# Kernel tuning notes

Hardware: AMD Instinct MI355X
Metric: run time of the kernel (lower is better)

## Reference

```python
import jax, jax.numpy as jnp
import numpy as np

N_NODES = 100000
N_EDGES = 800000
N_GRAPHS = 512          # 256 (query, corpus) pairs
NODE_FEAT, EDGE_FEAT = 16, 8
NODE_STATE, EDGE_STATE = 32, 16
MSG_H = 32              # message MLP hidden/out
UPD_H = 64              # node-update MLP hidden
GSTATE = 64             # graph embedding dim
N_PROP = 3
P = 1                   # int(output_mode[-1])
NODE_INS = NODE_DEL = 1.0


def _init_linear(key, fan_in, fan_out):
    s = 1.0 / np.sqrt(fan_in)
    kw, kb = jax.random.split(key)
    w = jax.random.uniform(kw, (fan_in, fan_out), jnp.float32, -s, s)
    b = jax.random.uniform(kb, (fan_out,), jnp.float32, -s, s)
    return w, b


def setup_inputs() -> dict:
    key = jax.random.key(0)
    ks = jax.random.split(key, 16)
    inp = {
        'node_features': jax.random.normal(ks[0], (N_NODES, NODE_FEAT), jnp.float32),
        'edge_features': jax.random.normal(ks[1], (N_EDGES, EDGE_FEAT), jnp.float32),
        'from_idx': jax.random.randint(ks[2], (N_EDGES,), 0, N_NODES, jnp.int32),
        'to_idx': jax.random.randint(ks[3], (N_EDGES,), 0, N_NODES, jnp.int32),
        'graph_idx': jnp.sort(jax.random.randint(ks[4], (N_NODES,), 0, N_GRAPHS, jnp.int32)),
    }
    # encoder (single linear layer MLPs, as in gmngen.GraphEncoder)
    inp['enc_node_w'], inp['enc_node_b'] = _init_linear(ks[5], NODE_FEAT, NODE_STATE)
    inp['enc_edge_w'], inp['enc_edge_b'] = _init_linear(ks[6], EDGE_FEAT, EDGE_STATE)
    # shared message net (reverse_dir_param_different=False): in = 2*node_state + edge_state
    inp['msg_w1'], inp['msg_b1'] = _init_linear(ks[7], 2 * NODE_STATE + EDGE_STATE, MSG_H)
    inp['msg_w2'], inp['msg_b2'] = _init_linear(ks[8], MSG_H, MSG_H)
    # residual node-update MLP: in = concat[agg_messages, node_states]
    inp['upd_w1'], inp['upd_b1'] = _init_linear(ks[9], MSG_H + NODE_STATE, UPD_H)
    inp['upd_w2'], inp['upd_b2'] = _init_linear(ks[10], UPD_H, NODE_STATE)
    # gated aggregator: MLP1 -> 2*GSTATE, MLP2: GSTATE -> GSTATE
    inp['agg_w1'], inp['agg_b1'] = _init_linear(ks[11], NODE_STATE, 2 * GSTATE)
    inp['agg_w2'], inp['agg_b2'] = _init_linear(ks[12], GSTATE, GSTATE)
    return inp


def _mlp2(x, w1, b1, w2, b2):
    return jax.nn.relu(x @ w1 + b1) @ w2 + b2


def reference(node_features, edge_features, from_idx, to_idx, graph_idx,
              enc_node_w, enc_node_b, enc_edge_w, enc_edge_b,
              msg_w1, msg_b1, msg_w2, msg_b2,
              upd_w1, upd_b1, upd_w2, upd_b2,
              agg_w1, agg_b1, agg_w2, agg_b2):
    # encoder
    h = node_features @ enc_node_w + enc_node_b              # [N, NODE_STATE]
    e = edge_features @ enc_edge_w + enc_edge_b              # [E, EDGE_STATE]

    for _ in range(N_PROP):
        fs = h[from_idx]                                     # [E, NODE_STATE]
        ts = h[to_idx]
        # forward-direction messages, scattered to to_idx
        m_f = _mlp2(jnp.concatenate([fs, ts, e], -1), msg_w1, msg_b1, msg_w2, msg_b2)
        agg = jax.ops.segment_sum(m_f, to_idx, num_segments=N_NODES)
        # reverse-direction messages (shared params), scattered to from_idx
        m_r = _mlp2(jnp.concatenate([ts, fs, e], -1), msg_w1, msg_b1, msg_w2, msg_b2)
        agg = agg + jax.ops.segment_sum(m_r, from_idx, num_segments=N_NODES)
        # residual node update: MLP(concat[messages, node_states]) + node_states
        h = h + _mlp2(jnp.concatenate([agg, h], -1), upd_w1, upd_b1, upd_w2, upd_b2)

    # gated aggregator
    g = h @ agg_w1 + agg_b1                                  # [N, 2*GSTATE]
    gated = jax.nn.sigmoid(g[:, :GSTATE]) * g[:, GSTATE:]
    graph_states = jax.ops.segment_sum(gated, graph_idx, num_segments=N_GRAPHS)
    graph_vectors = graph_states @ agg_w2 + agg_b2           # [G, GSTATE]

    # reshape_and_split_tensor(graph_vectors, 2): x = even rows, y = odd rows
    pairs = graph_vectors.reshape(-1, 2 * GSTATE)
    x, y = pairs[:, :GSTATE], pairs[:, GSTATE:]

    # asymm hinge norm, p = 1
    ins = jnp.sum(jax.nn.relu(y - x) ** P, axis=-1)
    dele = jnp.sum(jax.nn.relu(x - y) ** P, axis=-1)
    return NODE_INS * ins + NODE_DEL * dele                  # [G // 2]
```

## Files before the change

kernel.cpp:

```cpp
#include <hip/hip_runtime.h>
#include <math.h>

#define NN 100000
#define NE 800000
#define NG 512
#define NENT (2*NE)
#define NB ((NN + 1023)/1024)

__global__ __launch_bounds__(64) void k_prep(
    const float* __restrict__ ew, const float* __restrict__ eb,
    const float* __restrict__ mw1, const float* __restrict__ mb1,
    float* __restrict__ Wef, float* __restrict__ bef)
{
    int c = threadIdx.x;
    if (c >= 32) return;
    float bacc = mb1[c];
    for (int t = 0; t < 16; ++t) bacc = fmaf(eb[t], mw1[(64 + t) * 32 + c], bacc);
    bef[c] = bacc;
    for (int j = 0; j < 8; ++j) {
        float acc = 0.f;
        for (int t = 0; t < 16; ++t) acc = fmaf(ew[j * 16 + t], mw1[(64 + t) * 32 + c], acc);
        Wef[j * 32 + c] = acc;
    }
}

__global__ __launch_bounds__(256) void k_enc_nodes(
    const float* __restrict__ nf, const float* __restrict__ w,
    const float* __restrict__ bb, const float* __restrict__ mw1,
    float* __restrict__ h, float* __restrict__ A, float* __restrict__ B)
{
    int n = blockIdx.x * 256 + threadIdx.x;
    if (n >= NN) return;
    const float4* px = (const float4*)(nf + (size_t)n * 16);
    float4 x[4];
#pragma unroll
    for (int i = 0; i < 4; ++i) x[i] = px[i];
    float out[32];
#pragma unroll
    for (int j = 0; j < 32; ++j) out[j] = bb[j];
#pragma unroll
    for (int i = 0; i < 4; ++i) {
#pragma unroll
        for (int j = 0; j < 32; ++j) {
            out[j] = fmaf(x[i].x, w[(4*i+0)*32 + j], out[j]);
            out[j] = fmaf(x[i].y, w[(4*i+1)*32 + j], out[j]);
            out[j] = fmaf(x[i].z, w[(4*i+2)*32 + j], out[j]);
            out[j] = fmaf(x[i].w, w[(4*i+3)*32 + j], out[j]);
        }
    }
    float4* po = (float4*)(h + (size_t)n * 32);
#pragma unroll
    for (int j = 0; j < 8; ++j)
        po[j] = make_float4(out[4*j], out[4*j+1], out[4*j+2], out[4*j+3]);

    float Av[32], Bv[32];
#pragma unroll
    for (int c = 0; c < 32; ++c) { Av[c] = 0.f; Bv[c] = 0.f; }
#pragma unroll
    for (int i = 0; i < 32; ++i) {
        float r = out[i];
        const float* wra = mw1 + (size_t)i * 32;
        const float* wrb = mw1 + (size_t)(32 + i) * 32;
#pragma unroll
        for (int c = 0; c < 32; ++c) {
            Av[c] = fmaf(r, wra[c], Av[c]);
            Bv[c] = fmaf(r, wrb[c], Bv[c]);
        }
    }
    float4* pA = (float4*)(A + (size_t)n * 32);
    float4* pB = (float4*)(B + (size_t)n * 32);
#pragma unroll
    for (int j = 0; j < 8; ++j) {
        pA[j] = make_float4(Av[4*j], Av[4*j+1], Av[4*j+2], Av[4*j+3]);
        pB[j] = make_float4(Bv[4*j], Bv[4*j+1], Bv[4*j+2], Bv[4*j+3]);
    }
}

__global__ __launch_bounds__(256) void k_count(
    const int* __restrict__ fi, const int* __restrict__ ti, int* __restrict__ deg)
{
    int e = blockIdx.x * 256 + threadIdx.x;
    if (e >= NE) return;
    atomicAdd(&deg[ti[e]], 1);
    atomicAdd(&deg[fi[e]], 1);
}

__global__ __launch_bounds__(256) void k_scan1(
    const int* __restrict__ deg, int* __restrict__ offs, int* __restrict__ bsum)
{
    __shared__ int s[256];
    int b = blockIdx.x, t = threadIdx.x;
    int base = b * 1024 + t * 4;
    int v[4];
#pragma unroll
    for (int i = 0; i < 4; ++i) { int g = base + i; v[i] = (g < NN) ? deg[g] : 0; }
    int tsum = v[0] + v[1] + v[2] + v[3];
    s[t] = tsum;
    __syncthreads();
    for (int d = 1; d < 256; d <<= 1) {
        int xv = (t >= d) ? s[t - d] : 0;
        __syncthreads();
        s[t] += xv;
        __syncthreads();
    }
    int run = s[t] - tsum;
#pragma unroll
    for (int i = 0; i < 4; ++i) { int g = base + i; if (g < NN) offs[g] = run; run += v[i]; }
    if (t == 255) bsum[b] = s[255];
}

__global__ __launch_bounds__(128) void k_scan2(int* __restrict__ bsum, int nb)
{
    __shared__ int s[128];
    int t = threadIdx.x;
    int v = (t < nb) ? bsum[t] : 0;
    s[t] = v;
    __syncthreads();
    for (int d = 1; d < 128; d <<= 1) {
        int xv = (t >= d) ? s[t - d] : 0;
        __syncthreads();
        s[t] += xv;
        __syncthreads();
    }
    if (t < nb) bsum[t] = s[t] - v;
}

__global__ __launch_bounds__(256) void k_scan3(
    int* __restrict__ offs, const int* __restrict__ bsum, int* __restrict__ cursor)
{
    int g = blockIdx.x * 256 + threadIdx.x;
    if (g >= NN) return;
    int o = offs[g] + bsum[g >> 10];
    offs[g] = o;
    cursor[g] = o;
}

#define FILL_GROUPS 8
#define FILL_SUBBLK 256
#define RANGE_W (NN / FILL_GROUPS)
__global__ __launch_bounds__(256) void k_fill(
    const int* __restrict__ fi, const int* __restrict__ ti,
    int* __restrict__ cursor, int2* __restrict__ eplist)
{
    int grp = blockIdx.x & (FILL_GROUPS - 1);
    int sub = blockIdx.x >> 3;
    int lo = grp * RANGE_W;
    int hi = lo + RANGE_W;
    for (int e = sub * 256 + threadIdx.x; e < NE; e += FILL_SUBBLK * 256) {
        int f = fi[e], t = ti[e];
        if (t >= lo && t < hi) {
            int p = atomicAdd(&cursor[t], 1);
            eplist[p] = make_int2(e, f);
        }
        if (f >= lo && f < hi) {
            int p = atomicAdd(&cursor[f], 1);
            eplist[p] = make_int2(e, t);
        }
    }
}

__global__ __launch_bounds__(256) void k_gather(
    const int* __restrict__ offs, const int* __restrict__ deg,
    const int2* __restrict__ eplist,
    const float* __restrict__ A, const float* __restrict__ B,
    const float* __restrict__ ef,
    const float* __restrict__ Wef, const float* __restrict__ bef,
    float* __restrict__ aggH)
{
    int wave = (blockIdx.x * 256 + threadIdx.x) >> 6;
    if (wave >= NN) return;
    int lane = threadIdx.x & 63;
    int half = lane >> 5;
    int c = lane & 31;
    float w[8];
#pragma unroll
    for (int j = 0; j < 8; ++j) w[j] = Wef[j * 32 + c];
    float kbase = B[(size_t)wave * 32 + c] + bef[c];
    int beg = offs[wave];
    int end = beg + deg[wave];
    float acc0 = 0.f, acc1 = 0.f;
    int i = beg + half;
    for (; i + 2 < end; i += 4) {
        int2 ep0 = eplist[i];
        int2 ep1 = eplist[i + 2];
        float a0 = A[(size_t)ep0.y * 32 + c];
        float a1 = A[(size_t)ep1.y * 32 + c];
        const float4* pf0 = (const float4*)(ef + (size_t)ep0.x * 8);
        const float4* pf1 = (const float4*)(ef + (size_t)ep1.x * 8);
        float4 e00 = pf0[0], e01 = pf0[1];
        float4 e10 = pf1[0], e11 = pf1[1];
        float s0 = kbase + a0;
        s0 = fmaf(e00.x, w[0], s0); s0 = fmaf(e00.y, w[1], s0);
        s0 = fmaf(e00.z, w[2], s0); s0 = fmaf(e00.w, w[3], s0);
        s0 = fmaf(e01.x, w[4], s0); s0 = fmaf(e01.y, w[5], s0);
        s0 = fmaf(e01.z, w[6], s0); s0 = fmaf(e01.w, w[7], s0);
        float s1 = kbase + a1;
        s1 = fmaf(e10.x, w[0], s1); s1 = fmaf(e10.y, w[1], s1);
        s1 = fmaf(e10.z, w[2], s1); s1 = fmaf(e10.w, w[3], s1);
        s1 = fmaf(e11.x, w[4], s1); s1 = fmaf(e11.y, w[5], s1);
        s1 = fmaf(e11.z, w[6], s1); s1 = fmaf(e11.w, w[7], s1);
        acc0 += fmaxf(s0, 0.f);
        acc1 += fmaxf(s1, 0.f);
    }
    for (; i < end; i += 2) {
        int2 ep = eplist[i];
        float a = A[(size_t)ep.y * 32 + c];
        const float4* pf = (const float4*)(ef + (size_t)ep.x * 8);
        float4 f0 = pf[0], f1 = pf[1];
        float s = kbase + a;
        s = fmaf(f0.x, w[0], s); s = fmaf(f0.y, w[1], s);
        s = fmaf(f0.z, w[2], s); s = fmaf(f0.w, w[3], s);
        s = fmaf(f1.x, w[4], s); s = fmaf(f1.y, w[5], s);
        s = fmaf(f1.z, w[6], s); s = fmaf(f1.w, w[7], s);
        acc0 += fmaxf(s, 0.f);
    }
    float acc = acc0 + acc1;
    acc += __shfl_down(acc, 32);
    if (lane < 32) aggH[(size_t)wave * 32 + c] = acc;
}

__global__ __launch_bounds__(256) void k_update(
    const float* __restrict__ aggH, const int* __restrict__ deg,
    float* __restrict__ h,
    const float* __restrict__ mw2, const float* __restrict__ mb2,
    const float* __restrict__ uw1, const float* __restrict__ ub1,
    const float* __restrict__ uw2, const float* __restrict__ ub2,
    const float* __restrict__ mw1,
    float* __restrict__ A, float* __restrict__ B, int last)
{
    int n = blockIdx.x * 256 + threadIdx.x;
    if (n >= NN) return;
    float dg = (float)deg[n];
    float agg[32];
#pragma unroll
    for (int k = 0; k < 32; ++k) agg[k] = dg * mb2[k];
    {
        const float4* pa = (const float4*)(aggH + (size_t)n * 32);
#pragma unroll
        for (int i = 0; i < 8; ++i) {
            float4 v = pa[i];
            const float* wr0 = mw2 + (size_t)(4*i) * 32;
#pragma unroll
            for (int k = 0; k < 32; ++k) {
                float t0 = fmaf(v.x, wr0[k],      agg[k]);
                t0 = fmaf(v.y, wr0[32 + k], t0);
                t0 = fmaf(v.z, wr0[64 + k], t0);
                t0 = fmaf(v.w, wr0[96 + k], t0);
                agg[k] = t0;
            }
        }
    }
    float4* ph = (float4*)(h + (size_t)n * 32);
    float hv[32];
#pragma unroll
    for (int i = 0; i < 8; ++i) {
        float4 v = ph[i];
        hv[4*i] = v.x; hv[4*i+1] = v.y; hv[4*i+2] = v.z; hv[4*i+3] = v.w;
    }
    float out[32];
#pragma unroll
    for (int k = 0; k < 32; ++k) out[k] = ub2[k];
#pragma unroll
    for (int cB = 0; cB < 2; ++cB) {
        float hid[32];
#pragma unroll
        for (int j = 0; j < 32; ++j) hid[j] = ub1[cB * 32 + j];
#pragma unroll
        for (int i = 0; i < 32; ++i) {
            float r = agg[i];
            const float* wr = uw1 + (size_t)i * 64 + cB * 32;
#pragma unroll
            for (int j = 0; j < 32; ++j) hid[j] = fmaf(r, wr[j], hid[j]);
        }
#pragma unroll
        for (int i = 0; i < 32; ++i) {
            float r = hv[i];
            const float* wr = uw1 + (size_t)(32 + i) * 64 + cB * 32;
#pragma unroll
            for (int j = 0; j < 32; ++j) hid[j] = fmaf(r, wr[j], hid[j]);
        }
#pragma unroll
        for (int j = 0; j < 32; ++j) {
            float r = fmaxf(hid[j], 0.f);
            const float* wr = uw2 + (size_t)(cB * 32 + j) * 32;
#pragma unroll
            for (int k = 0; k < 32; ++k) out[k] = fmaf(r, wr[k], out[k]);
        }
    }
#pragma unroll
    for (int k = 0; k < 32; ++k) hv[k] += out[k];
#pragma unroll
    for (int i = 0; i < 8; ++i)
        ph[i] = make_float4(hv[4*i], hv[4*i+1], hv[4*i+2], hv[4*i+3]);

    if (!last) {
        float Av[32], Bv[32];
#pragma unroll
        for (int c = 0; c < 32; ++c) { Av[c] = 0.f; Bv[c] = 0.f; }
#pragma unroll
        for (int i = 0; i < 32; ++i) {
            float r = hv[i];
            const float* wra = mw1 + (size_t)i * 32;
            const float* wrb = mw1 + (size_t)(32 + i) * 32;
#pragma unroll
            for (int c = 0; c < 32; ++c) {
                Av[c] = fmaf(r, wra[c], Av[c]);
                Bv[c] = fmaf(r, wrb[c], Bv[c]);
            }
        }
        float4* pA = (float4*)(A + (size_t)n * 32);
        float4* pB = (float4*)(B + (size_t)n * 32);
#pragma unroll
        for (int j = 0; j < 8; ++j) {
            pA[j] = make_float4(Av[4*j], Av[4*j+1], Av[4*j+2], Av[4*j+3]);
            pB[j] = make_float4(Bv[4*j], Bv[4*j+1], Bv[4*j+2], Bv[4*j+3]);
        }
    }
}

#define FN_WAVES 4096
#define FN_CHUNK ((NN + FN_WAVES - 1) / FN_WAVES)
__global__ __launch_bounds__(256) void k_final_nodes(
    const float* __restrict__ h, const int* __restrict__ gidx,
    const float* __restrict__ w1, const float* __restrict__ b1,
    float* __restrict__ gs)
{
    int wid = (blockIdx.x * 256 + threadIdx.x) >> 6;
    int lane = threadIdx.x & 63;
    int beg = wid * FN_CHUNK;
    if (beg >= NN) return;
    int end = beg + FN_CHUNK; if (end > NN) end = NN;

    const float bl = b1[lane];
    const float bh = b1[64 + lane];
    float acc = 0.f;
    int curq = -1;
    for (int n = beg; n < end; ++n) {
        int q = gidx[n];
        if (q != curq) {
            if (curq >= 0 && acc != 0.f)
                atomicAdd(&gs[(size_t)curq * 64 + lane], acc);
            acc = 0.f;
            curq = q;
        }
        float xv = h[(size_t)n * 32 + (lane & 31)];
        float gl = bl, gh = bh;
#pragma unroll
        for (int i = 0; i < 32; ++i) {
            float xi = __shfl(xv, i);
            gl = fmaf(xi, w1[(size_t)i * 128 + lane],      gl);
            gh = fmaf(xi, w1[(size_t)i * 128 + 64 + lane], gh);
        }
        acc += gh / (1.0f + expf(-gl));
    }
    if (curq >= 0)
        atomicAdd(&gs[(size_t)curq * 64 + lane], acc);
}

__global__ __launch_bounds__(64) void k_pairs(
    const float* __restrict__ gs, const float* __restrict__ w2,
    const float* __restrict__ b2, float* __restrict__ out)
{
    int p = blockIdx.x;
    int k = threadIdx.x;
    const float* gx = gs + (size_t)(2*p) * 64;
    const float* gy = gs + (size_t)(2*p+1) * 64;
    float xk = b2[k], yk = b2[k];
    for (int i = 0; i < 64; ++i) {
        float w = w2[i*64 + k];
        xk = fmaf(gx[i], w, xk);
        yk = fmaf(gy[i], w, yk);
    }
    float d = fabsf(yk - xk);
#pragma unroll
    for (int s = 1; s < 64; s <<= 1) d += __shfl_xor(d, s);
    if (k == 0) out[p] = d;
}

extern "C" void kernel_launch(void* const* d_in, const int* in_sizes, int n_in,
                              void* d_out, int out_size, void* d_ws, size_t ws_size,
                              hipStream_t stream)
{
    const float* node_features = (const float*)d_in[0];
    const float* edge_features = (const float*)d_in[1];
    const int*   from_idx      = (const int*)d_in[2];
    const int*   to_idx        = (const int*)d_in[3];
    const int*   graph_idx     = (const int*)d_in[4];
    const float* enc_node_w = (const float*)d_in[5];
    const float* enc_node_b = (const float*)d_in[6];
    const float* enc_edge_w = (const float*)d_in[7];
    const float* enc_edge_b = (const float*)d_in[8];
    const float* msg_w1 = (const float*)d_in[9];
    const float* msg_b1 = (const float*)d_in[10];
    const float* msg_w2 = (const float*)d_in[11];
    const float* msg_b2 = (const float*)d_in[12];
    const float* upd_w1 = (const float*)d_in[13];
    const float* upd_b1 = (const float*)d_in[14];
    const float* upd_w2 = (const float*)d_in[15];
    const float* upd_b2 = (const float*)d_in[16];
    const float* agg_w1 = (const float*)d_in[17];
    const float* agg_b1 = (const float*)d_in[18];
    const float* agg_w2 = (const float*)d_in[19];
    const float* agg_b2 = (const float*)d_in[20];
    float* out = (float*)d_out;

    char* wsp = (char*)d_ws;
    auto alloc = [&](size_t bytes) {
        char* r = wsp;
        wsp += (bytes + 255) & ~(size_t)255;
        return r;
    };
    float* h     = (float*)alloc((size_t)NN * 32 * 4);
    float* A     = (float*)alloc((size_t)NN * 32 * 4);
    float* B     = (float*)alloc((size_t)NN * 32 * 4);
    float* aggH  = (float*)alloc((size_t)NN * 32 * 4);
    float* gs    = (float*)alloc((size_t)NG * 64 * 4);
    int*   deg   = (int*)alloc((size_t)NN * 4);
    int*   offs  = (int*)alloc((size_t)NN * 4);
    int*   cursor= (int*)alloc((size_t)NN * 4);
    int2*  eplist= (int2*)alloc(((size_t)NENT + 16) * 8);
    int*   bsum  = (int*)alloc(128 * 4);
    float* Wef   = (float*)alloc(8 * 32 * 4);
    float* bef   = (float*)alloc(32 * 4);

    hipMemsetAsync(deg, 0, (size_t)NN * 4, stream);

    k_prep<<<1, 64, 0, stream>>>(enc_edge_w, enc_edge_b, msg_w1, msg_b1, Wef, bef);
    k_enc_nodes<<<(NN + 255) / 256, 256, 0, stream>>>(node_features, enc_node_w,
                                                      enc_node_b, msg_w1, h, A, B);

    k_count<<<NE / 256, 256, 0, stream>>>(from_idx, to_idx, deg);
    k_scan1<<<NB, 256, 0, stream>>>(deg, offs, bsum);
    k_scan2<<<1, 128, 0, stream>>>(bsum, NB);
    k_scan3<<<(NN + 255) / 256, 256, 0, stream>>>(offs, bsum, cursor);
    k_fill<<<FILL_GROUPS * FILL_SUBBLK, 256, 0, stream>>>(from_idx, to_idx, cursor, eplist);

    for (int it = 0; it < 3; ++it) {
        k_gather<<<NN / 4, 256, 0, stream>>>(offs, deg, eplist, A, B,
                                             edge_features, Wef, bef, aggH);
        k_update<<<(NN + 255) / 256, 256, 0, stream>>>(aggH, deg, h,
                                                       msg_w2, msg_b2,
                                                       upd_w1, upd_b1,
                                                       upd_w2, upd_b2,
                                                       msg_w1, A, B, it == 2);
    }

    hipMemsetAsync(gs, 0, (size_t)NG * 64 * 4, stream);
    k_final_nodes<<<FN_WAVES / 4, 256, 0, stream>>>(h, graph_idx, agg_w1, agg_b1, gs);
    k_pairs<<<NG / 2, 64, 0, stream>>>(gs, agg_w2, agg_b2, out);
}
```

Before: 897.9 us.

## Split node-update MLP across two threads per node with LDS exchange

The node-update kernel now gives each node to two threads, each computing half of the 64-wide hidden layer and one of the two A/B projections, with partial outputs combined through shared memory. This doubles the thread count and halves per-thread serial FMA work and register pressure, aimed at the low occupancy of the original one-thread-per-node kernel. Weight loads are also vectorised to float4. In exchange, the message MLP layer (mw2) is computed redundantly by both threads, and the kernel adds a 33KB shared buffer and a block barrier.

```diff
diff --git a/kernel.cpp b/kernel.cpp
--- a/kernel.cpp
+++ b/kernel.cpp
@@ -219,6 +219,8 @@
     if (lane < 32) aggH[(size_t)wave * 32 + c] = acc;
 }
 
+#define UPD_NPB 128
+#define UPD_GRID ((NN + UPD_NPB - 1) / UPD_NPB)
 __global__ __launch_bounds__(256) void k_update(
     const float* __restrict__ aggH, const int* __restrict__ deg,
     float* __restrict__ h,
@@ -228,92 +230,125 @@
     const float* __restrict__ mw1,
     float* __restrict__ A, float* __restrict__ B, int last)
 {
-    int n = blockIdx.x * 256 + threadIdx.x;
-    if (n >= NN) return;
+    __shared__ float xch[256][33];
+    int tl  = threadIdx.x & 127;
+    int p   = threadIdx.x >> 7;
+    int nid = blockIdx.x * UPD_NPB + tl;
+    bool valid = nid < NN;
+    int n = valid ? nid : (NN - 1);
+
+    float av[32], hv[32];
+    {
+        const float4* pa  = (const float4*)(aggH + (size_t)n * 32);
+        const float4* phv = (const float4*)(h + (size_t)n * 32);
+#pragma unroll
+        for (int i = 0; i < 8; ++i) {
+            float4 v = pa[i];
+            av[4*i] = v.x; av[4*i+1] = v.y; av[4*i+2] = v.z; av[4*i+3] = v.w;
+            float4 u = phv[i];
+            hv[4*i] = u.x; hv[4*i+1] = u.y; hv[4*i+2] = u.z; hv[4*i+3] = u.w;
+        }
+    }
     float dg = (float)deg[n];
     float agg[32];
 #pragma unroll
     for (int k = 0; k < 32; ++k) agg[k] = dg * mb2[k];
-    {
-        const float4* pa = (const float4*)(aggH + (size_t)n * 32);
-#pragma unroll
-        for (int i = 0; i < 8; ++i) {
-            float4 v = pa[i];
-            const float* wr0 = mw2 + (size_t)(4*i) * 32;
-#pragma unroll
-            for (int k = 0; k < 32; ++k) {
-                float t0 = fmaf(v.x, wr0[k],      agg[k]);
-                t0 = fmaf(v.y, wr0[32 + k], t0);
-                t0 = fmaf(v.z, wr0[64 + k], t0);
-                t0 = fmaf(v.w, wr0[96 + k], t0);
-                agg[k] = t0;
+#pragma unroll
+    for (int i = 0; i < 32; ++i) {
+        float r = av[i];
+        const float4* wr = (const float4*)(mw2 + (size_t)i * 32);
+#pragma unroll
+        for (int k4 = 0; k4 < 8; ++k4) {
+            float4 wv = wr[k4];
+            agg[4*k4]   = fmaf(r, wv.x, agg[4*k4]);
+            agg[4*k4+1] = fmaf(r, wv.y, agg[4*k4+1]);
+            agg[4*k4+2] = fmaf(r, wv.z, agg[4*k4+2]);
+            agg[4*k4+3] = fmaf(r, wv.w, agg[4*k4+3]);
+        }
+    }
+    float hid[32];
+#pragma unroll
+    for (int j = 0; j < 32; ++j) hid[j] = ub1[p * 32 + j];
+#pragma unroll
+    for (int i = 0; i < 32; ++i) {
+        float r = agg[i];
+        const float4* wr = (const float4*)(uw1 + (size_t)i * 64 + p * 32);
+#pragma unroll
+        for (int j4 = 0; j4 < 8; ++j4) {
+            float4 wv = wr[j4];
+            hid[4*j4]   = fmaf(r, wv.x, hid[4*j4]);
+            hid[4*j4+1] = fmaf(r, wv.y, hid[4*j4+1]);
+            hid[4*j4+2] = fmaf(r, wv.z, hid[4*j4+2]);
+            hid[4*j4+3] = fmaf(r, wv.w, hid[4*j4+3]);
+        }
+    }
+#pragma unroll
+    for (int i = 0; i < 32; ++i) {
+        float r = hv[i];
+        const float4* wr = (const float4*)(uw1 + (size_t)(32 + i) * 64 + p * 32);
+#pragma unroll
+        for (int j4 = 0; j4 < 8; ++j4) {
+            float4 wv = wr[j4];
+            hid[4*j4]   = fmaf(r, wv.x, hid[4*j4]);
+            hid[4*j4+1] = fmaf(r, wv.y, hid[4*j4+1]);
+            hid[4*j4+2] = fmaf(r, wv.z, hid[4*j4+2]);
+            hid[4*j4+3] = fmaf(r, wv.w, hid[4*j4+3]);
+        }
+    }
+    float outp[32];
+#pragma unroll
+    for (int k = 0; k < 32; ++k) outp[k] = 0.f;
+#pragma unroll
+    for (int j = 0; j < 32; ++j) {
+        float r = fmaxf(hid[j], 0.f);
+        const float4* wr = (const float4*)(uw2 + (size_t)(p * 32 + j) * 32);
+#pragma unroll
+        for (int k4 = 0; k4 < 8; ++k4) {
+            float4 wv = wr[k4];
+            outp[4*k4]   = fmaf(r, wv.x, outp[4*k4]);
+            outp[4*k4+1] = fmaf(r, wv.y, outp[4*k4+1]);
+            outp[4*k4+2] = fmaf(r, wv.z, outp[4*k4+2]);
+            outp[4*k4+3] = fmaf(r, wv.w, outp[4*k4+3]);
+        }
+    }
+#pragma unroll
+    for (int k = 0; k < 32; ++k) xch[threadIdx.x][k] = outp[k];
+    __syncthreads();
+    const float* part = xch[threadIdx.x ^ 128];
+    float hnew[32];
+#pragma unroll
+    for (int k = 0; k < 32; ++k)
+        hnew[k] = hv[k] + outp[k] + part[k] + ub2[k];
+
+    if (valid) {
+        if (p == 0) {
+            float4* ph = (float4*)(h + (size_t)n * 32);
+#pragma unroll
+            for (int i = 0; i < 8; ++i)
+                ph[i] = make_float4(hnew[4*i], hnew[4*i+1], hnew[4*i+2], hnew[4*i+3]);
+        }
+        if (!last) {
+            float acc[32];
+#pragma unroll
+            for (int c = 0; c < 32; ++c) acc[c] = 0.f;
+            const float* wbase = mw1 + (size_t)(p * 32) * 32;
+#pragma unroll
+            for (int i = 0; i < 32; ++i) {
+                float r = hnew[i];
+                const float4* wr = (const float4*)(wbase + (size_t)i * 32);
+#pragma unroll
+                for (int c4 = 0; c4 < 8; ++c4) {
+                    float4 wv = wr[c4];
+                    acc[4*c4]   = fmaf(r, wv.x, acc[4*c4]);
+                    acc[4*c4+1] = fmaf(r, wv.y, acc[4*c4+1]);
+                    acc[4*c4+2] = fmaf(r, wv.z, acc[4*c4+2]);
+                    acc[4*c4+3] = fmaf(r, wv.w, acc[4*c4+3]);
+                }
             }
-        }
-    }
-    float4* ph = (float4*)(h + (size_t)n * 32);
-    float hv[32];
-#pragma unroll
-    for (int i = 0; i < 8; ++i) {
-        float4 v = ph[i];
-        hv[4*i] = v.x; hv[4*i+1] = v.y; hv[4*i+2] = v.z; hv[4*i+3] = v.w;
-    }
-    float out[32];
-#pragma unroll
-    for (int k = 0; k < 32; ++k) out[k] = ub2[k];
-#pragma unroll
-    for (int cB = 0; cB < 2; ++cB) {
-        float hid[32];
-#pragma unroll
-        for (int j = 0; j < 32; ++j) hid[j] = ub1[cB * 32 + j];
-#pragma unroll
-        for (int i = 0; i < 32; ++i) {
-            float r = agg[i];
-            const float* wr = uw1 + (size_t)i * 64 + cB * 32;
-#pragma unroll
-            for (int j = 0; j < 32; ++j) hid[j] = fmaf(r, wr[j], hid[j]);
-        }
-#pragma unroll
-        for (int i = 0; i < 32; ++i) {
-            float r = hv[i];
-            const float* wr = uw1 + (size_t)(32 + i) * 64 + cB * 32;
-#pragma unroll
-            for (int j = 0; j < 32; ++j) hid[j] = fmaf(r, wr[j], hid[j]);
-        }
-#pragma unroll
-        for (int j = 0; j < 32; ++j) {
-            float r = fmaxf(hid[j], 0.f);
-            const float* wr = uw2 + (size_t)(cB * 32 + j) * 32;
-#pragma unroll
-            for (int k = 0; k < 32; ++k) out[k] = fmaf(r, wr[k], out[k]);
-        }
-    }
-#pragma unroll
-    for (int k = 0; k < 32; ++k) hv[k] += out[k];
-#pragma unroll
-    for (int i = 0; i < 8; ++i)
-        ph[i] = make_float4(hv[4*i], hv[4*i+1], hv[4*i+2], hv[4*i+3]);
-
-    if (!last) {
-        float Av[32], Bv[32];
-#pragma unroll
-        for (int c = 0; c < 32; ++c) { Av[c] = 0.f; Bv[c] = 0.f; }
-#pragma unroll
-        for (int i = 0; i < 32; ++i) {
-            float r = hv[i];
-            const float* wra = mw1 + (size_t)i * 32;
-            const float* wrb = mw1 + (size_t)(32 + i) * 32;
-#pragma unroll
-            for (int c = 0; c < 32; ++c) {
-                Av[c] = fmaf(r, wra[c], Av[c]);
-                Bv[c] = fmaf(r, wrb[c], Bv[c]);
-            }
-        }
-        float4* pA = (float4*)(A + (size_t)n * 32);
-        float4* pB = (float4*)(B + (size_t)n * 32);
-#pragma unroll
-        for (int j = 0; j < 8; ++j) {
-            pA[j] = make_float4(Av[4*j], Av[4*j+1], Av[4*j+2], Av[4*j+3]);
-            pB[j] = make_float4(Bv[4*j], Bv[4*j+1], Bv[4*j+2], Bv[4*j+3]);
+            float4* pd = (float4*)((p == 0 ? A : B) + (size_t)n * 32);
+#pragma unroll
+            for (int i = 0; i < 8; ++i)
+                pd[i] = make_float4(acc[4*i], acc[4*i+1], acc[4*i+2], acc[4*i+3]);
         }
     }
 }
@@ -438,11 +473,11 @@
     for (int it = 0; it < 3; ++it) {
         k_gather<<<NN / 4, 256, 0, stream>>>(offs, deg, eplist, A, B,
                                              edge_features, Wef, bef, aggH);
-        k_update<<<(NN + 255) / 256, 256, 0, stream>>>(aggH, deg, h,
-                                                       msg_w2, msg_b2,
-                                                       upd_w1, upd_b1,
-                                                       upd_w2, upd_b2,
-                                                       msg_w1, A, B, it == 2);
+        k_update<<<UPD_GRID, 256, 0, stream>>>(aggH, deg, h,
+                                               msg_w2, msg_b2,
+                                               upd_w1, upd_b1,
+                                               upd_w2, upd_b2,
+                                               msg_w1, A, B, it == 2);
     }
 
     hipMemsetAsync(gs, 0, (size_t)NG * 64 * 4, stream);
```

After: 991.3 us. 1.1x slower.

## Fold msg_w2 into update weights and restructure node update as wave-per-node

Applied to the files above, without the earlier changes.

Precomputes M1 = msg_w2 @ upd_w1[:32] and c1 = msg_b2 @ upd_w1[:32] in the prep kernel, so the node update skips the separate 32x32 message-output matmul. The update kernel moves from one thread per node with large register arrays to one wave per node, each lane holding one column of weights in registers. Hidden and output values are broadcast across lanes with readlane. This cuts FLOPs and register pressure, but each node is now processed serially within a wave and every weight is reloaded per wave.

```diff
diff --git a/kernel.cpp b/kernel.cpp
--- a/kernel.cpp
+++ b/kernel.cpp
@@ -7,20 +7,37 @@
 #define NENT (2*NE)
 #define NB ((NN + 1023)/1024)
 
+__device__ __forceinline__ float rlane(float v, int l) {
+    return __int_as_float(__builtin_amdgcn_readlane(__float_as_int(v), l));
+}
+
 __global__ __launch_bounds__(64) void k_prep(
     const float* __restrict__ ew, const float* __restrict__ eb,
     const float* __restrict__ mw1, const float* __restrict__ mb1,
-    float* __restrict__ Wef, float* __restrict__ bef)
-{
-    int c = threadIdx.x;
-    if (c >= 32) return;
-    float bacc = mb1[c];
-    for (int t = 0; t < 16; ++t) bacc = fmaf(eb[t], mw1[(64 + t) * 32 + c], bacc);
-    bef[c] = bacc;
-    for (int j = 0; j < 8; ++j) {
+    const float* __restrict__ mw2, const float* __restrict__ mb2,
+    const float* __restrict__ uw1,
+    float* __restrict__ Wef, float* __restrict__ bef,
+    float* __restrict__ M1, float* __restrict__ c1)
+{
+    int j = threadIdx.x;
+    float cacc = 0.f;
+    for (int t = 0; t < 32; ++t) cacc = fmaf(mb2[t], uw1[t * 64 + j], cacc);
+    c1[j] = cacc;
+    for (int i = 0; i < 32; ++i) {
         float acc = 0.f;
-        for (int t = 0; t < 16; ++t) acc = fmaf(ew[j * 16 + t], mw1[(64 + t) * 32 + c], acc);
-        Wef[j * 32 + c] = acc;
+        for (int t = 0; t < 32; ++t) acc = fmaf(mw2[i * 32 + t], uw1[t * 64 + j], acc);
+        M1[i * 64 + j] = acc;
+    }
+    if (j < 32) {
+        int c = j;
+        float bacc = mb1[c];
+        for (int t = 0; t < 16; ++t) bacc = fmaf(eb[t], mw1[(64 + t) * 32 + c], bacc);
+        bef[c] = bacc;
+        for (int jj = 0; jj < 8; ++jj) {
+            float acc = 0.f;
+            for (int t = 0; t < 16; ++t) acc = fmaf(ew[jj * 16 + t], mw1[(64 + t) * 32 + c], acc);
+            Wef[jj * 32 + c] = acc;
+        }
     }
 }
 
@@ -219,101 +236,78 @@
     if (lane < 32) aggH[(size_t)wave * 32 + c] = acc;
 }
 
+#define U3_WAVES 2048
+#define U3_CHUNK ((NN + U3_WAVES - 1) / U3_WAVES)
 __global__ __launch_bounds__(256) void k_update(
     const float* __restrict__ aggH, const int* __restrict__ deg,
     float* __restrict__ h,
-    const float* __restrict__ mw2, const float* __restrict__ mb2,
+    const float* __restrict__ M1, const float* __restrict__ c1,
     const float* __restrict__ uw1, const float* __restrict__ ub1,
     const float* __restrict__ uw2, const float* __restrict__ ub2,
     const float* __restrict__ mw1,
     float* __restrict__ A, float* __restrict__ B, int last)
 {
-    int n = blockIdx.x * 256 + threadIdx.x;
-    if (n >= NN) return;
-    float dg = (float)deg[n];
-    float agg[32];
-#pragma unroll
-    for (int k = 0; k < 32; ++k) agg[k] = dg * mb2[k];
-    {
+    int wid = __builtin_amdgcn_readfirstlane((int)((blockIdx.x * 256 + threadIdx.x) >> 6));
+    int lane = threadIdx.x & 63;
+    int c = lane & 31;
+    int half = lane >> 5;
+    int n0 = wid * U3_CHUNK;
+    if (n0 >= NN) return;
+    int n1 = n0 + U3_CHUNK; if (n1 > NN) n1 = NN;
+
+    float wM[32], wU[32], w2f[64], w1r[32];
+#pragma unroll
+    for (int i = 0; i < 32; ++i) wM[i] = M1[i * 64 + lane];
+#pragma unroll
+    for (int i = 0; i < 32; ++i) wU[i] = uw1[(size_t)(32 + i) * 64 + lane];
+#pragma unroll
+    for (int j = 0; j < 64; ++j) w2f[j] = uw2[(size_t)j * 32 + c];
+#pragma unroll
+    for (int i = 0; i < 32; ++i) w1r[i] = mw1[(size_t)(half * 32 + i) * 32 + c];
+    const float blane = ub1[lane];
+    const float c1l = c1[lane];
+    const float b2c = ub2[c];
+
+    for (int n = n0; n < n1; ++n) {
         const float4* pa = (const float4*)(aggH + (size_t)n * 32);
-#pragma unroll
-        for (int i = 0; i < 8; ++i) {
-            float4 v = pa[i];
-            const float* wr0 = mw2 + (size_t)(4*i) * 32;
-#pragma unroll
-            for (int k = 0; k < 32; ++k) {
-                float t0 = fmaf(v.x, wr0[k],      agg[k]);
-                t0 = fmaf(v.y, wr0[32 + k], t0);
-                t0 = fmaf(v.z, wr0[64 + k], t0);
-                t0 = fmaf(v.w, wr0[96 + k], t0);
-                agg[k] = t0;
+        const float4* ph = (const float4*)(h + (size_t)n * 32);
+        float dg = (float)deg[n];
+        float hc = h[(size_t)n * 32 + c];
+        float h0 = fmaf(dg, c1l, blane), h1 = 0.f;
+#pragma unroll
+        for (int q = 0; q < 8; ++q) {
+            float4 va = pa[q];
+            h0 = fmaf(va.x, wM[4*q+0], h0);
+            h1 = fmaf(va.y, wM[4*q+1], h1);
+            h0 = fmaf(va.z, wM[4*q+2], h0);
+            h1 = fmaf(va.w, wM[4*q+3], h1);
+        }
+#pragma unroll
+        for (int q = 0; q < 8; ++q) {
+            float4 vh = ph[q];
+            h0 = fmaf(vh.x, wU[4*q+0], h0);
+            h1 = fmaf(vh.y, wU[4*q+1], h1);
+            h0 = fmaf(vh.z, wU[4*q+2], h0);
+            h1 = fmaf(vh.w, wU[4*q+3], h1);
+        }
+        float hr = fmaxf(h0 + h1, 0.f);
+        float o0 = 0.f, o1 = 0.f;
+#pragma unroll
+        for (int j = 0; j < 64; j += 2) {
+            o0 = fmaf(rlane(hr, j),     w2f[j],     o0);
+            o1 = fmaf(rlane(hr, j + 1), w2f[j + 1], o1);
+        }
+        float hnew = hc + o0 + o1 + b2c;
+        if (lane < 32) h[(size_t)n * 32 + lane] = hnew;
+        if (!last) {
+            float a0 = 0.f, a1 = 0.f;
+#pragma unroll
+            for (int i = 0; i < 32; i += 2) {
+                a0 = fmaf(rlane(hnew, i),     w1r[i],     a0);
+                a1 = fmaf(rlane(hnew, i + 1), w1r[i + 1], a1);
             }
-        }
-    }
-    float4* ph = (float4*)(h + (size_t)n * 32);
-    float hv[32];
-#pragma unroll
-    for (int i = 0; i < 8; ++i) {
-        float4 v = ph[i];
-        hv[4*i] = v.x; hv[4*i+1] = v.y; hv[4*i+2] = v.z; hv[4*i+3] = v.w;
-    }
-    float out[32];
-#pragma unroll
-    for (int k = 0; k < 32; ++k) out[k] = ub2[k];
-#pragma unroll
-    for (int cB = 0; cB < 2; ++cB) {
-        float hid[32];
-#pragma unroll
-        for (int j = 0; j < 32; ++j) hid[j] = ub1[cB * 32 + j];
-#pragma unroll
-        for (int i = 0; i < 32; ++i) {
-            float r = agg[i];
-            const float* wr = uw1 + (size_t)i * 64 + cB * 32;
-#pragma unroll
-            for (int j = 0; j < 32; ++j) hid[j] = fmaf(r, wr[j], hid[j]);
-        }
-#pragma unroll
-        for (int i = 0; i < 32; ++i) {
-            float r = hv[i];
-            const float* wr = uw1 + (size_t)(32 + i) * 64 + cB * 32;
-#pragma unroll
-            for (int j = 0; j < 32; ++j) hid[j] = fmaf(r, wr[j], hid[j]);
-        }
-#pragma unroll
-        for (int j = 0; j < 32; ++j) {
-            float r = fmaxf(hid[j], 0.f);
-            const float* wr = uw2 + (size_t)(cB * 32 + j) * 32;
-#pragma unroll
-            for (int k = 0; k < 32; ++k) out[k] = fmaf(r, wr[k], out[k]);
-        }
-    }
-#pragma unroll
-    for (int k = 0; k < 32; ++k) hv[k] += out[k];
-#pragma unroll
-    for (int i = 0; i < 8; ++i)
-        ph[i] = make_float4(hv[4*i], hv[4*i+1], hv[4*i+2], hv[4*i+3]);
-
-    if (!last) {
-        float Av[32], Bv[32];
-#pragma unroll
-        for (int c = 0; c < 32; ++c) { Av[c] = 0.f; Bv[c] = 0.f; }
-#pragma unroll
-        for (int i = 0; i < 32; ++i) {
-            float r = hv[i];
-            const float* wra = mw1 + (size_t)i * 32;
-            const float* wrb = mw1 + (size_t)(32 + i) * 32;
-#pragma unroll
-            for (int c = 0; c < 32; ++c) {
-                Av[c] = fmaf(r, wra[c], Av[c]);
-                Bv[c] = fmaf(r, wrb[c], Bv[c]);
-            }
-        }
-        float4* pA = (float4*)(A + (size_t)n * 32);
-        float4* pB = (float4*)(B + (size_t)n * 32);
-#pragma unroll
-        for (int j = 0; j < 8; ++j) {
-            pA[j] = make_float4(Av[4*j], Av[4*j+1], Av[4*j+2], Av[4*j+3]);
-            pB[j] = make_float4(Bv[4*j], Bv[4*j+1], Bv[4*j+2], Bv[4*j+3]);
+            float* dst = (half == 0) ? A : B;
+            dst[(size_t)n * 32 + c] = a0 + a1;
         }
     }
 }
@@ -422,10 +416,13 @@
     int*   bsum  = (int*)alloc(128 * 4);
     float* Wef   = (float*)alloc(8 * 32 * 4);
     float* bef   = (float*)alloc(32 * 4);
+    float* M1    = (float*)alloc(32 * 64 * 4);
+    float* c1    = (float*)alloc(64 * 4);
 
     hipMemsetAsync(deg, 0, (size_t)NN * 4, stream);
 
-    k_prep<<<1, 64, 0, stream>>>(enc_edge_w, enc_edge_b, msg_w1, msg_b1, Wef, bef);
+    k_prep<<<1, 64, 0, stream>>>(enc_edge_w, enc_edge_b, msg_w1, msg_b1,
+                                 msg_w2, msg_b2, upd_w1, Wef, bef, M1, c1);
     k_enc_nodes<<<(NN + 255) / 256, 256, 0, stream>>>(node_features, enc_node_w,
                                                       enc_node_b, msg_w1, h, A, B);
 
@@ -438,11 +435,11 @@
     for (int it = 0; it < 3; ++it) {
         k_gather<<<NN / 4, 256, 0, stream>>>(offs, deg, eplist, A, B,
                                              edge_features, Wef, bef, aggH);
-        k_update<<<(NN + 255) / 256, 256, 0, stream>>>(aggH, deg, h,
-                                                       msg_w2, msg_b2,
-                                                       upd_w1, upd_b1,
-                                                       upd_w2, upd_b2,
-                                                       msg_w1, A, B, it == 2);
+        k_update<<<U3_WAVES / 4, 256, 0, stream>>>(aggH, deg, h,
+                                                   M1, c1,
+                                                   upd_w1, upd_b1,
+                                                   upd_w2, upd_b2,
+                                                   msg_w1, A, B, it == 2);
     }
 
     hipMemsetAsync(gs, 0, (size_t)NG * 64 * 4, stream);
```

Result: faster. 839.8 us (-6.5%).
